# Kernel tuning notes

Measured on AMD Instinct MI355X. Metric: run time of the kernel, lower is better.

## Reference

```python
import jax, jax.numpy as jnp
import numpy as np

DIM = 192
HEADS = 6
WS = 8                      # window size (Wh = Ww = 8)
N = WS * WS                 # tokens per window = 64
NW = 1024                   # windows per image (256/8)^2
BATCH = 2
B_ = NW * BATCH             # 2048 windows total
TABLE = (2 * WS - 1) ** 2   # 225 relative-position entries


def _relative_position_index():
    coords = np.stack(np.meshgrid(np.arange(WS), np.arange(WS), indexing='ij'))  # (2,WS,WS)
    cf = coords.reshape(2, -1)                       # (2, N)
    rc = (cf[:, :, None] - cf[:, None, :]).transpose(1, 2, 0).astype(np.int64)  # (N,N,2)
    rc[..., 0] += WS - 1
    rc[..., 1] += WS - 1
    rc[..., 0] *= 2 * WS - 1
    return rc.sum(-1)                                # (N, N) in [0, TABLE)


def setup_inputs() -> dict:
    key = jax.random.key(0)
    ks = jax.random.split(key, 16)
    s = 0.02
    inp = {
        'x': jax.random.normal(ks[0], (B_, N, DIM), jnp.float32),
        'y': jax.random.normal(ks[1], (B_, N, DIM), jnp.float32),
        'mask_x': jnp.zeros((NW, N, N), jnp.float32),
        'mask_y': jnp.zeros((NW, N, N), jnp.float32),
        'qkv_w': jax.random.normal(ks[2], (3 * DIM, DIM), jnp.float32) * s,
        'qkv_b': jnp.zeros((3 * DIM,), jnp.float32),
        'kv_w': jax.random.normal(ks[3], (2 * DIM, DIM), jnp.float32) * s,
        'kv_b': jnp.zeros((2 * DIM,), jnp.float32),
        'rpb_x': jax.random.normal(ks[4], (TABLE, HEADS), jnp.float32) * s,
        'rpb_y': jax.random.normal(ks[5], (TABLE, HEADS), jnp.float32) * s,
        'merge1_w': jax.random.normal(ks[6], (DIM, 2 * DIM), jnp.float32) * s,
        'merge1_b': jnp.zeros((DIM,), jnp.float32),
        'merge2_w': jax.random.normal(ks[7], (DIM, DIM), jnp.float32) * s,
        'merge2_b': jnp.zeros((DIM,), jnp.float32),
        'proj_w': jax.random.normal(ks[8], (DIM, DIM), jnp.float32) * s,
        'proj_b': jnp.zeros((DIM,), jnp.float32),
        'rel_idx': jnp.asarray(_relative_position_index(), jnp.int32),
    }
    return inp


def _attend(q, k, v, table, rel_idx, mask):
    # q,k,v: (B_, H, N, hd); table: (TABLE, H); mask: (nW, N, N)
    b_, h, n, hd = q.shape
    bias = table[rel_idx].transpose(2, 0, 1)                 # (H, N, N)
    attn = jnp.einsum('bhnd,bhmd->bhnm', q, k) + bias[None]  # (B_, H, N, N)
    nW = mask.shape[0]
    attn = attn.reshape(b_ // nW, nW, h, n, n) + mask[None, :, None]
    attn = jax.nn.softmax(attn.reshape(b_, h, n, n), axis=-1)
    out = jnp.einsum('bhnm,bhmd->bhnd', attn, v)             # (B_, H, N, hd)
    return out.transpose(0, 2, 1, 3).reshape(b_, n, h * hd)


def reference(x, y, mask_x, mask_y, qkv_w, qkv_b, kv_w, kv_b, rpb_x, rpb_y,
              merge1_w, merge1_b, merge2_w, merge2_b, proj_w, proj_b, rel_idx):
    b_, n, c = x.shape
    hd = c // HEADS
    scale = hd ** (-0.5)
    qkv = (x @ qkv_w.T + qkv_b).reshape(b_, n, 3, HEADS, hd).transpose(2, 0, 3, 1, 4)
    q, k, v = qkv[0] * scale, qkv[1], qkv[2]
    x_self = _attend(q, k, v, rpb_x, rel_idx, mask_x)
    kv = (y @ kv_w.T + kv_b).reshape(b_, n, 2, HEADS, hd).transpose(2, 0, 3, 1, 4)
    x_cross = _attend(q, kv[0], kv[1], rpb_y, rel_idx, mask_y)
    m = jnp.concatenate([x_self, x_cross], axis=-1) @ merge1_w.T + merge1_b
    m = jax.nn.leaky_relu(m, negative_slope=0.2)
    m = m @ merge2_w.T + merge2_b
    return m @ proj_w.T + proj_b
```

## Files before the change

### kernel.cpp

```cpp
#include <hip/hip_runtime.h>

#define DEVINL __device__ __forceinline__

typedef __attribute__((ext_vector_type(8))) short          s16x8;
typedef __attribute__((ext_vector_type(8))) unsigned short u16x8;
typedef __attribute__((ext_vector_type(4))) unsigned short u16x4;
typedef __attribute__((ext_vector_type(4))) float          f32x4;

DEVINL unsigned short f2b(float f) {
    union { float f; unsigned int u; } c; c.f = f;
    return (unsigned short)((c.u + 0x7FFFu + ((c.u >> 16) & 1u)) >> 16);
}
DEVINL f32x4 mfma16(s16x8 a, s16x8 b, f32x4 c) {
    return __builtin_amdgcn_mfma_f32_16x16x32_bf16(a, b, c, 0, 0, 0);
}

#define QKV_ELEMS 110592
#define KV_ELEMS  73728
#define M1_ELEMS  73728
#define M2_ELEMS  36864
#define PW_ELEMS  36864
#define O_QKV 0
#define O_KV  110592
#define O_M1  184320
#define O_M2  258048
#define O_PW  294912
#define WB_ELEMS 331776
#define WB_BYTES (WB_ELEMS * 2)

#define LD_IN  200
#define LD_K   200
#define LD_VT  72
#define LD_P   72
#define LD_CAT 392
#define LD_M   200
#define OFF_IN 0
#define OFF_Q  12800
#define OFF_K  25600
#define OFF_VT 38400
#define OFF_P  52224
#define SMEM_ELEMS 61440
#define CATB OFF_Q
#define M1B  OFF_IN
#define M2B  OFF_VT

#define SCALE 0.17677669529663687f
#define LOG2E 1.4426950408889634f

__global__ __launch_bounds__(256) void cvt_w(
    const float* __restrict__ a, const float* __restrict__ b, const float* __restrict__ c,
    const float* __restrict__ d, const float* __restrict__ e, unsigned short* __restrict__ o)
{
    int i = (blockIdx.x * 256 + threadIdx.x) * 4;
    if (i >= WB_ELEMS) return;
    const float* s; int off;
    if (i < O_KV)      { s = a; off = i - O_QKV; }
    else if (i < O_M1) { s = b; off = i - O_KV; }
    else if (i < O_M2) { s = c; off = i - O_M1; }
    else if (i < O_PW) { s = d; off = i - O_M2; }
    else               { s = e; off = i - O_PW; }
    float4 v = *(const float4*)(s + off);
    u16x4 r;
    r[0] = f2b(v.x); r[1] = f2b(v.y); r[2] = f2b(v.z); r[3] = f2b(v.w);
    *(u16x4*)(o + i) = r;
}

template<bool WB>
DEVINL s16x8 loadB(const unsigned short* wbp, const float* wfp, int off) {
    if constexpr (WB) {
        return *(const s16x8*)(wbp + off);
    } else {
        float4 v0 = *(const float4*)(wfp + off);
        float4 v1 = *(const float4*)(wfp + off + 4);
        s16x8 r;
        r[0] = (short)f2b(v0.x); r[1] = (short)f2b(v0.y); r[2] = (short)f2b(v0.z); r[3] = (short)f2b(v0.w);
        r[4] = (short)f2b(v1.x); r[5] = (short)f2b(v1.y); r[6] = (short)f2b(v1.z); r[7] = (short)f2b(v1.w);
        return r;
    }
}

template<bool WB>
__global__ __launch_bounds__(512, 2) void swin_fused(
    const float* __restrict__ x,
    const float* __restrict__ y,
    const float* __restrict__ mask_x,
    const float* __restrict__ mask_y,
    const float* __restrict__ qkv_w,
    const float* __restrict__ qkv_b,
    const float* __restrict__ kv_w,
    const float* __restrict__ kv_b,
    const float* __restrict__ rpb_x,
    const float* __restrict__ rpb_y,
    const float* __restrict__ m1w,
    const float* __restrict__ m1b,
    const float* __restrict__ m2w,
    const float* __restrict__ m2b,
    const float* __restrict__ pw,
    const float* __restrict__ pb,
    const int* __restrict__ rel_idx,
    const unsigned short* __restrict__ wb,
    float* __restrict__ out)
{
    __shared__ __align__(16) unsigned short smem[SMEM_ELEMS];

    const int tid  = threadIdx.x;
    const int w    = tid >> 6;
    const int lane = tid & 63;
    const int l16  = lane & 15;
    const int quad = lane >> 4;
    const int wm   = w >> 2;
    const int wn   = w & 3;
    const int rb   = w >> 1;
    const int hh   = w & 1;
    const int b    = blockIdx.x;
    const int widx = b & 1023;

    const unsigned short* wqkv = WB ? wb + O_QKV : nullptr;
    const unsigned short* wkv  = WB ? wb + O_KV  : nullptr;
    const unsigned short* wm1  = WB ? wb + O_M1  : nullptr;
    const unsigned short* wm2  = WB ? wb + O_M2  : nullptr;
    const unsigned short* wpw  = WB ? wb + O_PW  : nullptr;

    {
        const float4* gx = (const float4*)(x + (size_t)b * 64 * 192);
        #pragma unroll
        for (int it = 0; it < 3; ++it) {
            int c = it * 512 + tid;
            int e = c * 8;
            int row = e / 192, col = e - row * 192;
            float4 v0 = gx[c * 2], v1 = gx[c * 2 + 1];
            u16x8 r;
            r[0] = f2b(v0.x); r[1] = f2b(v0.y); r[2] = f2b(v0.z); r[3] = f2b(v0.w);
            r[4] = f2b(v1.x); r[5] = f2b(v1.y); r[6] = f2b(v1.z); r[7] = f2b(v1.w);
            *(u16x8*)&smem[OFF_IN + row * LD_IN + col] = r;
        }
    }
    __syncthreads();

    {
        s16x8 afr[2][6];
        #pragma unroll
        for (int mt = 0; mt < 2; ++mt)
            #pragma unroll
            for (int ks = 0; ks < 6; ++ks)
                afr[mt][ks] = *(const s16x8*)&smem[OFF_IN + (wm * 32 + mt * 16 + l16) * LD_IN + ks * 32 + quad * 8];

        #pragma unroll
        for (int nt = 0; nt < 9; ++nt) {
            int n0  = wn * 144 + nt * 16;
            int col = n0 + l16;
            f32x4 acc0 = {0,0,0,0}, acc1 = {0,0,0,0};
            #pragma unroll
            for (int ks = 0; ks < 6; ++ks) {
                s16x8 bf = loadB<WB>(wqkv, qkv_w, col * 192 + ks * 32 + quad * 8);
                acc0 = mfma16(afr[0][ks], bf, acc0);
                acc1 = mfma16(afr[1][ks], bf, acc1);
            }
            f32x4 accv[2] = {acc0, acc1};
            float bias = qkv_b[col];
            if (n0 < 192) {
                #pragma unroll
                for (int mt = 0; mt < 2; ++mt)
                    #pragma unroll
                    for (int r = 0; r < 4; ++r)
                        smem[OFF_Q + (wm * 32 + mt * 16 + quad * 4 + r) * LD_K + col] =
                            f2b((accv[mt][r] + bias) * SCALE);
            } else if (n0 < 384) {
                #pragma unroll
                for (int mt = 0; mt < 2; ++mt)
                    #pragma unroll
                    for (int r = 0; r < 4; ++r)
                        smem[OFF_K + (wm * 32 + mt * 16 + quad * 4 + r) * LD_K + (col - 192)] =
                            f2b(accv[mt][r] + bias);
            } else {
                #pragma unroll
                for (int mt = 0; mt < 2; ++mt)
                    #pragma unroll
                    for (int r = 0; r < 4; ++r)
                        smem[OFF_VT + (col - 384) * LD_VT + (wm * 32 + mt * 16 + quad * 4 + r)] =
                            f2b(accv[mt][r] + bias);
            }
        }
    }
    __syncthreads();

    {
        const float4* gy = (const float4*)(y + (size_t)b * 64 * 192);
        #pragma unroll
        for (int it = 0; it < 3; ++it) {
            int c = it * 512 + tid;
            int e = c * 8;
            int row = e / 192, col = e - row * 192;
            float4 v0 = gy[c * 2], v1 = gy[c * 2 + 1];
            u16x8 r;
            r[0] = f2b(v0.x); r[1] = f2b(v0.y); r[2] = f2b(v0.z); r[3] = f2b(v0.w);
            r[4] = f2b(v1.x); r[5] = f2b(v1.y); r[6] = f2b(v1.z); r[7] = f2b(v1.w);
            *(u16x8*)&smem[OFF_IN + row * LD_IN + col] = r;
        }
    }

    int idxv[16];
    #pragma unroll
    for (int i = 0; i < 16; ++i) {
        int ntt = i >> 2, r = i & 3;
        int row = rb * 16 + quad * 4 + r;
        int col = ntt * 16 + l16;
        idxv[i] = rel_idx[row * 64 + col];
    }

    auto do_attn = [&](const float* __restrict__ rpb,
                       const float* __restrict__ mask,
                       f32x4 (&oacc)[3][2]) {
        float maskv[16];
        #pragma unroll
        for (int i = 0; i < 16; ++i) {
            int ntt = i >> 2, r = i & 3;
            int row = rb * 16 + quad * 4 + r;
            int col = ntt * 16 + l16;
            maskv[i] = mask[(size_t)widx * 4096 + row * 64 + col];
        }
        const int pbase = OFF_P + w * 16 * LD_P;
        #pragma unroll
        for (int hl = 0; hl < 3; ++hl) {
            int h = hh * 3 + hl;
            s16x8 aQ = *(const s16x8*)&smem[OFF_Q + (rb * 16 + l16) * LD_K + h * 32 + quad * 8];
            f32x4 sacc[4];
            #pragma unroll
            for (int ntt = 0; ntt < 4; ++ntt) {
                s16x8 bK = *(const s16x8*)&smem[OFF_K + (ntt * 16 + l16) * LD_K + h * 32 + quad * 8];
                f32x4 z = {0,0,0,0};
                sacc[ntt] = mfma16(aQ, bK, z);
            }
            float sv[4][4];
            #pragma unroll
            for (int ntt = 0; ntt < 4; ++ntt)
                #pragma unroll
                for (int r = 0; r < 4; ++r)
                    sv[ntt][r] = sacc[ntt][r] + rpb[idxv[ntt * 4 + r] * 6 + h] + maskv[ntt * 4 + r];
            float pv[4][4];
            #pragma unroll
            for (int r = 0; r < 4; ++r) {
                float mx = fmaxf(fmaxf(sv[0][r], sv[1][r]), fmaxf(sv[2][r], sv[3][r]));
                mx = fmaxf(mx, __shfl_xor(mx, 1));
                mx = fmaxf(mx, __shfl_xor(mx, 2));
                mx = fmaxf(mx, __shfl_xor(mx, 4));
                mx = fmaxf(mx, __shfl_xor(mx, 8));
                float e0 = __builtin_amdgcn_exp2f((sv[0][r] - mx) * LOG2E);
                float e1 = __builtin_amdgcn_exp2f((sv[1][r] - mx) * LOG2E);
                float e2 = __builtin_amdgcn_exp2f((sv[2][r] - mx) * LOG2E);
                float e3 = __builtin_amdgcn_exp2f((sv[3][r] - mx) * LOG2E);
                float s = e0 + e1 + e2 + e3;
                s += __shfl_xor(s, 1);
                s += __shfl_xor(s, 2);
                s += __shfl_xor(s, 4);
                s += __shfl_xor(s, 8);
                float inv = __builtin_amdgcn_rcpf(s);
                pv[0][r] = e0 * inv; pv[1][r] = e1 * inv; pv[2][r] = e2 * inv; pv[3][r] = e3 * inv;
            }
            #pragma unroll
            for (int ntt = 0; ntt < 4; ++ntt)
                #pragma unroll
                for (int r = 0; r < 4; ++r)
                    smem[pbase + (quad * 4 + r) * LD_P + ntt * 16 + l16] = f2b(pv[ntt][r]);
            #pragma unroll
            for (int nd = 0; nd < 2; ++nd) {
                f32x4 o = oacc[hl][nd];
                #pragma unroll
                for (int kt = 0; kt < 2; ++kt) {
                    s16x8 aP = *(const s16x8*)&smem[pbase + l16 * LD_P + kt * 32 + quad * 8];
                    s16x8 bV = *(const s16x8*)&smem[OFF_VT + (h * 32 + nd * 16 + l16) * LD_VT + kt * 32 + quad * 8];
                    o = mfma16(aP, bV, o);
                }
                oacc[hl][nd] = o;
            }
        }
    };

    f32x4 os[3][2];
    #pragma unroll
    for (int hl = 0; hl < 3; ++hl) { f32x4 z = {0,0,0,0}; os[hl][0] = z; os[hl][1] = z; }
    do_attn(rpb_x, mask_x, os);
    __syncthreads();

    {
        s16x8 afr[2][6];
        #pragma unroll
        for (int mt = 0; mt < 2; ++mt)
            #pragma unroll
            for (int ks = 0; ks < 6; ++ks)
                afr[mt][ks] = *(const s16x8*)&smem[OFF_IN + (wm * 32 + mt * 16 + l16) * LD_IN + ks * 32 + quad * 8];

        #pragma unroll
        for (int nt = 0; nt < 6; ++nt) {
            int n0  = wn * 96 + nt * 16;
            int col = n0 + l16;
            f32x4 acc0 = {0,0,0,0}, acc1 = {0,0,0,0};
            #pragma unroll
            for (int ks = 0; ks < 6; ++ks) {
                s16x8 bf = loadB<WB>(wkv, kv_w, col * 192 + ks * 32 + quad * 8);
                acc0 = mfma16(afr[0][ks], bf, acc0);
                acc1 = mfma16(afr[1][ks], bf, acc1);
            }
            f32x4 accv[2] = {acc0, acc1};
            float bias = kv_b[col];
            if (n0 < 192) {
                #pragma unroll
                for (int mt = 0; mt < 2; ++mt)
                    #pragma unroll
                    for (int r = 0; r < 4; ++r)
                        smem[OFF_K + (wm * 32 + mt * 16 + quad * 4 + r) * LD_K + col] =
                            f2b(accv[mt][r] + bias);
            } else {
                #pragma unroll
                for (int mt = 0; mt < 2; ++mt)
                    #pragma unroll
                    for (int r = 0; r < 4; ++r)
                        smem[OFF_VT + (col - 192) * LD_VT + (wm * 32 + mt * 16 + quad * 4 + r)] =
                            f2b(accv[mt][r] + bias);
            }
        }
    }
    __syncthreads();

    f32x4 oc[3][2];
    #pragma unroll
    for (int hl = 0; hl < 3; ++hl) { f32x4 z = {0,0,0,0}; oc[hl][0] = z; oc[hl][1] = z; }
    do_attn(rpb_y, mask_y, oc);
    __syncthreads();

    #pragma unroll
    for (int hl = 0; hl < 3; ++hl) {
        int h = hh * 3 + hl;
        #pragma unroll
        for (int nd = 0; nd < 2; ++nd)
            #pragma unroll
            for (int r = 0; r < 4; ++r) {
                int row = rb * 16 + quad * 4 + r;
                int c0  = h * 32 + nd * 16 + l16;
                smem[CATB + row * LD_CAT + c0]       = f2b(os[hl][nd][r]);
                smem[CATB + row * LD_CAT + 192 + c0] = f2b(oc[hl][nd][r]);
            }
    }
    __syncthreads();

    {
        s16x8 cfr[2][12];
        #pragma unroll
        for (int mt = 0; mt < 2; ++mt)
            #pragma unroll
            for (int ks = 0; ks < 12; ++ks)
                cfr[mt][ks] = *(const s16x8*)&smem[CATB + (wm * 32 + mt * 16 + l16) * LD_CAT + ks * 32 + quad * 8];

        #pragma unroll
        for (int nt = 0; nt < 3; ++nt) {
            int n0  = wn * 48 + nt * 16;
            int col = n0 + l16;
            f32x4 acc0 = {0,0,0,0}, acc1 = {0,0,0,0};
            #pragma unroll
            for (int ks = 0; ks < 12; ++ks) {
                s16x8 bf = loadB<WB>(wm1, m1w, col * 384 + ks * 32 + quad * 8);
                acc0 = mfma16(cfr[0][ks], bf, acc0);
                acc1 = mfma16(cfr[1][ks], bf, acc1);
            }
            f32x4 accv[2] = {acc0, acc1};
            float bias = m1b[col];
            #pragma unroll
            for (int mt = 0; mt < 2; ++mt)
                #pragma unroll
                for (int r = 0; r < 4; ++r) {
                    float v = accv[mt][r] + bias;
                    v = (v > 0.f) ? v : 0.2f * v;
                    smem[M1B + (wm * 32 + mt * 16 + quad * 4 + r) * LD_M + col] = f2b(v);
                }
        }
    }
    __syncthreads();

    {
        s16x8 afr[2][6];
        #pragma unroll
        for (int mt = 0; mt < 2; ++mt)
            #pragma unroll
            for (int ks = 0; ks < 6; ++ks)
                afr[mt][ks] = *(const s16x8*)&smem[M1B + (wm * 32 + mt * 16 + l16) * LD_M + ks * 32 + quad * 8];

        #pragma unroll
        for (int nt = 0; nt < 3; ++nt) {
            int n0  = wn * 48 + nt * 16;
            int col = n0 + l16;
            f32x4 acc0 = {0,0,0,0}, acc1 = {0,0,0,0};
            #pragma unroll
            for (int ks = 0; ks < 6; ++ks) {
                s16x8 bf = loadB<WB>(wm2, m2w, col * 192 + ks * 32 + quad * 8);
                acc0 = mfma16(afr[0][ks], bf, acc0);
                acc1 = mfma16(afr[1][ks], bf, acc1);
            }
            f32x4 accv[2] = {acc0, acc1};
            float bias = m2b[col];
            #pragma unroll
            for (int mt = 0; mt < 2; ++mt)
                #pragma unroll
                for (int r = 0; r < 4; ++r)
                    smem[M2B + (wm * 32 + mt * 16 + quad * 4 + r) * LD_M + col] = f2b(accv[mt][r] + bias);
        }
    }
    __syncthreads();

    {
        s16x8 afr[2][6];
        #pragma unroll
        for (int mt = 0; mt < 2; ++mt)
            #pragma unroll
            for (int ks = 0; ks < 6; ++ks)
                afr[mt][ks] = *(const s16x8*)&smem[M2B + (wm * 32 + mt * 16 + l16) * LD_M + ks * 32 + quad * 8];

        #pragma unroll
        for (int nt = 0; nt < 3; ++nt) {
            int n0  = wn * 48 + nt * 16;
            int col = n0 + l16;
            f32x4 acc0 = {0,0,0,0}, acc1 = {0,0,0,0};
            #pragma unroll
            for (int ks = 0; ks < 6; ++ks) {
                s16x8 bf = loadB<WB>(wpw, pw, col * 192 + ks * 32 + quad * 8);
                acc0 = mfma16(afr[0][ks], bf, acc0);
                acc1 = mfma16(afr[1][ks], bf, acc1);
            }
            f32x4 accv[2] = {acc0, acc1};
            float bias = pb[col];
            #pragma unroll
            for (int mt = 0; mt < 2; ++mt)
                #pragma unroll
                for (int r = 0; r < 4; ++r) {
                    int row = wm * 32 + mt * 16 + quad * 4 + r;
                    out[((size_t)b * 64 + row) * 192 + col] = accv[mt][r] + bias;
                }
        }
    }
}

extern "C" void kernel_launch(void* const* d_in, const int* in_sizes, int n_in,
                              void* d_out, int out_size, void* d_ws, size_t ws_size,
                              hipStream_t stream) {
    (void)in_sizes; (void)n_in; (void)out_size;
    const float* x    = (const float*)d_in[0];
    const float* y    = (const float*)d_in[1];
    const float* mx   = (const float*)d_in[2];
    const float* my   = (const float*)d_in[3];
    const float* qw   = (const float*)d_in[4];
    const float* qb   = (const float*)d_in[5];
    const float* kw   = (const float*)d_in[6];
    const float* kb   = (const float*)d_in[7];
    const float* rx   = (const float*)d_in[8];
    const float* ry   = (const float*)d_in[9];
    const float* m1w  = (const float*)d_in[10];
    const float* m1b  = (const float*)d_in[11];
    const float* m2w  = (const float*)d_in[12];
    const float* m2b  = (const float*)d_in[13];
    const float* pw   = (const float*)d_in[14];
    const float* pb   = (const float*)d_in[15];
    const int*   ridx = (const int*)d_in[16];
    float* out = (float*)d_out;

    if (ws_size >= (size_t)WB_BYTES) {
        unsigned short* wbuf = (unsigned short*)d_ws;
        cvt_w<<<WB_ELEMS / 4 / 256, 256, 0, stream>>>(qw, kw, m1w, m2w, pw, wbuf);
        swin_fused<true><<<2048, 512, 0, stream>>>(
            x, y, mx, my, qw, qb, kw, kb, rx, ry, m1w, m1b, m2w, m2b, pw, pb, ridx,
            wbuf, out);
    } else {
        swin_fused<false><<<2048, 512, 0, stream>>>(
            x, y, mx, my, qw, qb, kw, kb, rx, ry, m1w, m1b, m2w, m2b, pw, pb, ridx,
            nullptr, out);
    }
}
```

Before: 645.6 us.

## Alias shared-memory regions to cut LDS footprint and raise occupancy target

Rearranges the shared-memory plan so the input tile, Q, P scratch and merge buffers reuse three regions instead of five, shrinking the LDS footprint from about 120 KB to about 77 KB per block. Q fragments are preloaded into registers so the Q region can be reused as P scratch. The y-tile load moves to after self-attention, and extra barriers guard the reuse. Launch bounds now ask for 4 blocks of 512 threads per CU instead of 2, aiming for more resident waves at the cost of a tighter register budget, possible spills, and lost overlap of the y load with compute.

```diff
diff --git a/kernel.cpp b/kernel.cpp
--- a/kernel.cpp
+++ b/kernel.cpp
@@ -34,15 +34,11 @@
 #define LD_P   72
 #define LD_CAT 392
 #define LD_M   200
-#define OFF_IN 0
-#define OFF_Q  12800
-#define OFF_K  25600
-#define OFF_VT 38400
-#define OFF_P  52224
-#define SMEM_ELEMS 61440
-#define CATB OFF_Q
-#define M1B  OFF_IN
-#define M2B  OFF_VT
+#define OFF_R1 0
+#define OFF_R2 12800
+#define OFF_R3 25600
+#define SMEM_ELEMS 39424
+#define CATB OFF_R2
 
 #define SCALE 0.17677669529663687f
 #define LOG2E 1.4426950408889634f
@@ -80,7 +76,7 @@
 }
 
 template<bool WB>
-__global__ __launch_bounds__(512, 2) void swin_fused(
+__global__ __launch_bounds__(512, 4) void swin_fused(
     const float* __restrict__ x,
     const float* __restrict__ y,
     const float* __restrict__ mask_x,
@@ -132,7 +128,7 @@
             u16x8 r;
             r[0] = f2b(v0.x); r[1] = f2b(v0.y); r[2] = f2b(v0.z); r[3] = f2b(v0.w);
             r[4] = f2b(v1.x); r[5] = f2b(v1.y); r[6] = f2b(v1.z); r[7] = f2b(v1.w);
-            *(u16x8*)&smem[OFF_IN + row * LD_IN + col] = r;
+            *(u16x8*)&smem[OFF_R1 + row * LD_IN + col] = r;
         }
     }
     __syncthreads();
@@ -143,7 +139,8 @@
         for (int mt = 0; mt < 2; ++mt)
             #pragma unroll
             for (int ks = 0; ks < 6; ++ks)
-                afr[mt][ks] = *(const s16x8*)&smem[OFF_IN + (wm * 32 + mt * 16 + l16) * LD_IN + ks * 32 + quad * 8];
+                afr[mt][ks] = *(const s16x8*)&smem[OFF_R1 + (wm * 32 + mt * 16 + l16) * LD_IN + ks * 32 + quad * 8];
+        __syncthreads();
 
         #pragma unroll
         for (int nt = 0; nt < 9; ++nt) {
@@ -163,41 +160,32 @@
                 for (int mt = 0; mt < 2; ++mt)
                     #pragma unroll
                     for (int r = 0; r < 4; ++r)
-                        smem[OFF_Q + (wm * 32 + mt * 16 + quad * 4 + r) * LD_K + col] =
+                        smem[OFF_R1 + (wm * 32 + mt * 16 + quad * 4 + r) * LD_K + col] =
                             f2b((accv[mt][r] + bias) * SCALE);
             } else if (n0 < 384) {
                 #pragma unroll
                 for (int mt = 0; mt < 2; ++mt)
                     #pragma unroll
                     for (int r = 0; r < 4; ++r)
-                        smem[OFF_K + (wm * 32 + mt * 16 + quad * 4 + r) * LD_K + (col - 192)] =
+                        smem[OFF_R2 + (wm * 32 + mt * 16 + quad * 4 + r) * LD_K + (col - 192)] =
                             f2b(accv[mt][r] + bias);
             } else {
                 #pragma unroll
                 for (int mt = 0; mt < 2; ++mt)
                     #pragma unroll
                     for (int r = 0; r < 4; ++r)
-                        smem[OFF_VT + (col - 384) * LD_VT + (wm * 32 + mt * 16 + quad * 4 + r)] =
+                        smem[OFF_R3 + (col - 384) * LD_VT + (wm * 32 + mt * 16 + quad * 4 + r)] =
                             f2b(accv[mt][r] + bias);
             }
         }
     }
     __syncthreads();
 
-    {
-        const float4* gy = (const float4*)(y + (size_t)b * 64 * 192);
-        #pragma unroll
-        for (int it = 0; it < 3; ++it) {
-            int c = it * 512 + tid;
-            int e = c * 8;
-            int row = e / 192, col = e - row * 192;
-            float4 v0 = gy[c * 2], v1 = gy[c * 2 + 1];
-            u16x8 r;
-            r[0] = f2b(v0.x); r[1] = f2b(v0.y); r[2] = f2b(v0.z); r[3] = f2b(v0.w);
-            r[4] = f2b(v1.x); r[5] = f2b(v1.y); r[6] = f2b(v1.z); r[7] = f2b(v1.w);
-            *(u16x8*)&smem[OFF_IN + row * LD_IN + col] = r;
-        }
-    }
+    s16x8 aQ[3];
+    #pragma unroll
+    for (int hl = 0; hl < 3; ++hl)
+        aQ[hl] = *(const s16x8*)&smem[OFF_R1 + (rb * 16 + l16) * LD_K + (hh * 3 + hl) * 32 + quad * 8];
+    __syncthreads();
 
     int idxv[16];
     #pragma unroll
@@ -219,17 +207,16 @@
             int col = ntt * 16 + l16;
             maskv[i] = mask[(size_t)widx * 4096 + row * 64 + col];
         }
-        const int pbase = OFF_P + w * 16 * LD_P;
+        const int pbase = OFF_R1 + w * 16 * LD_P;
         #pragma unroll
         for (int hl = 0; hl < 3; ++hl) {
             int h = hh * 3 + hl;
-            s16x8 aQ = *(const s16x8*)&smem[OFF_Q + (rb * 16 + l16) * LD_K + h * 32 + quad * 8];
             f32x4 sacc[4];
             #pragma unroll
             for (int ntt = 0; ntt < 4; ++ntt) {
-                s16x8 bK = *(const s16x8*)&smem[OFF_K + (ntt * 16 + l16) * LD_K + h * 32 + quad * 8];
+                s16x8 bK = *(const s16x8*)&smem[OFF_R2 + (ntt * 16 + l16) * LD_K + h * 32 + quad * 8];
                 f32x4 z = {0,0,0,0};
-                sacc[ntt] = mfma16(aQ, bK, z);
+                sacc[ntt] = mfma16(aQ[hl], bK, z);
             }
             float sv[4][4];
             #pragma unroll
@@ -268,7 +255,7 @@
                 #pragma unroll
                 for (int kt = 0; kt < 2; ++kt) {
                     s16x8 aP = *(const s16x8*)&smem[pbase + l16 * LD_P + kt * 32 + quad * 8];
-                    s16x8 bV = *(const s16x8*)&smem[OFF_VT + (h * 32 + nd * 16 + l16) * LD_VT + kt * 32 + quad * 8];
+                    s16x8 bV = *(const s16x8*)&smem[OFF_R3 + (h * 32 + nd * 16 + l16) * LD_VT + kt * 32 + quad * 8];
                     o = mfma16(aP, bV, o);
                 }
                 oacc[hl][nd] = o;
@@ -283,12 +270,28 @@
     __syncthreads();
 
     {
+        const float4* gy = (const float4*)(y + (size_t)b * 64 * 192);
+        #pragma unroll
+        for (int it = 0; it < 3; ++it) {
+            int c = it * 512 + tid;
+            int e = c * 8;
+            int row = e / 192, col = e - row * 192;
+            float4 v0 = gy[c * 2], v1 = gy[c * 2 + 1];
+            u16x8 r;
+            r[0] = f2b(v0.x); r[1] = f2b(v0.y); r[2] = f2b(v0.z); r[3] = f2b(v0.w);
+            r[4] = f2b(v1.x); r[5] = f2b(v1.y); r[6] = f2b(v1.z); r[7] = f2b(v1.w);
+            *(u16x8*)&smem[OFF_R1 + row * LD_IN + col] = r;
+        }
+    }
+    __syncthreads();
+
+    {
         s16x8 afr[2][6];
         #pragma unroll
         for (int mt = 0; mt < 2; ++mt)
             #pragma unroll
             for (int ks = 0; ks < 6; ++ks)
-                afr[mt][ks] = *(const s16x8*)&smem[OFF_IN + (wm * 32 + mt * 16 + l16) * LD_IN + ks * 32 + quad * 8];
+                afr[mt][ks] = *(const s16x8*)&smem[OFF_R1 + (wm * 32 + mt * 16 + l16) * LD_IN + ks * 32 + quad * 8];
 
         #pragma unroll
         for (int nt = 0; nt < 6; ++nt) {
@@ -308,14 +311,14 @@
                 for (int mt = 0; mt < 2; ++mt)
                     #pragma unroll
                     for (int r = 0; r < 4; ++r)
-                        smem[OFF_K + (wm * 32 + mt * 16 + quad * 4 + r) * LD_K + col] =
+                        smem[OFF_R2 + (wm * 32 + mt * 16 + quad * 4 + r) * LD_K + col] =
                             f2b(accv[mt][r] + bias);
             } else {
                 #pragma unroll
                 for (int mt = 0; mt < 2; ++mt)
                     #pragma unroll
                     for (int r = 0; r < 4; ++r)
-                        smem[OFF_VT + (col - 192) * LD_VT + (wm * 32 + mt * 16 + quad * 4 + r)] =
+                        smem[OFF_R3 + (col - 192) * LD_VT + (wm * 32 + mt * 16 + quad * 4 + r)] =
                             f2b(accv[mt][r] + bias);
             }
         }
@@ -370,7 +373,7 @@
                 for (int r = 0; r < 4; ++r) {
                     float v = accv[mt][r] + bias;
                     v = (v > 0.f) ? v : 0.2f * v;
-                    smem[M1B + (wm * 32 + mt * 16 + quad * 4 + r) * LD_M + col] = f2b(v);
+                    smem[OFF_R1 + (wm * 32 + mt * 16 + quad * 4 + r) * LD_M + col] = f2b(v);
                 }
         }
     }
@@ -382,7 +385,7 @@
         for (int mt = 0; mt < 2; ++mt)
             #pragma unroll
             for (int ks = 0; ks < 6; ++ks)
-                afr[mt][ks] = *(const s16x8*)&smem[M1B + (wm * 32 + mt * 16 + l16) * LD_M + ks * 32 + quad * 8];
+                afr[mt][ks] = *(const s16x8*)&smem[OFF_R1 + (wm * 32 + mt * 16 + l16) * LD_M + ks * 32 + quad * 8];
 
         #pragma unroll
         for (int nt = 0; nt < 3; ++nt) {
@@ -401,7 +404,7 @@
             for (int mt = 0; mt < 2; ++mt)
                 #pragma unroll
                 for (int r = 0; r < 4; ++r)
-                    smem[M2B + (wm * 32 + mt * 16 + quad * 4 + r) * LD_M + col] = f2b(accv[mt][r] + bias);
+                    smem[OFF_R2 + (wm * 32 + mt * 16 + quad * 4 + r) * LD_M + col] = f2b(accv[mt][r] + bias);
         }
     }
     __syncthreads();
@@ -412,7 +415,7 @@
         for (int mt = 0; mt < 2; ++mt)
             #pragma unroll
             for (int ks = 0; ks < 6; ++ks)
-                afr[mt][ks] = *(const s16x8*)&smem[M2B + (wm * 32 + mt * 16 + l16) * LD_M + ks * 32 + quad * 8];
+                afr[mt][ks] = *(const s16x8*)&smem[OFF_R2 + (wm * 32 + mt * 16 + l16) * LD_M + ks * 32 + quad * 8];
 
         #pragma unroll
         for (int nt = 0; nt < 3; ++nt) {
```

New measurement: 635.7 us. Within noise of the previous version (-1.5%).
